# Optimization experiments

Measured on AMD Instinct MI355X. Metric: run time of the kernel, lower is better.

## Reference

```python
import jax, jax.numpy as jnp
import numpy as np

B, S, D, H, A = 4, 2048, 512, 8, 64


def setup_inputs() -> dict:
    key = jax.random.key(0)
    ks = jax.random.split(key, 12)
    inv_d = 1.0 / np.sqrt(D)
    inv_ha = 1.0 / np.sqrt(H * A)
    return {
        "query": jax.random.normal(ks[0], (B, S, D), jnp.float32),
        "key": jax.random.normal(ks[1], (B, S, D), jnp.float32),
        "value": jax.random.normal(ks[2], (B, S, D), jnp.float32),
        # stacked per-head projection weights, layout [H, in, out] so y = x @ W + b
        "Wq": jax.random.uniform(ks[3], (H, D, A), jnp.float32, -inv_d, inv_d),
        "bq": jax.random.uniform(ks[4], (H, A), jnp.float32, -inv_d, inv_d),
        "Wk": jax.random.uniform(ks[5], (H, D, A), jnp.float32, -inv_d, inv_d),
        "bk": jax.random.uniform(ks[6], (H, A), jnp.float32, -inv_d, inv_d),
        "Wv": jax.random.uniform(ks[7], (H, D, A), jnp.float32, -inv_d, inv_d),
        "bv": jax.random.uniform(ks[8], (H, A), jnp.float32, -inv_d, inv_d),
        "Wo": jax.random.uniform(ks[9], (H * A, D), jnp.float32, -inv_ha, inv_ha),
        "bo": jax.random.uniform(ks[10], (D,), jnp.float32, -inv_ha, inv_ha),
    }


def reference(query, key, value, Wq, bq, Wk, bk, Wv, bv, Wo, bo):
    b, s, _ = query.shape
    h, _, a = Wq.shape
    # per-head projections, batched across heads: [B,H,S,A]
    q = jnp.einsum("bsd,hda->bhsa", query, Wq) + bq[None, :, None, :]
    k = jnp.einsum("bsd,hda->bhsa", key, Wk) + bk[None, :, None, :]
    v = jnp.einsum("bsd,hda->bhsa", value, Wv) + bv[None, :, None, :]
    scale = a ** 0.5
    scores = jnp.einsum("bhqa,bhka->bhqk", q, k) / scale  # [B,H,S,S]
    # Faithful to original: subsequent_mask has 0.0 on lower tri, -inf above;
    # masked_fill(mask == 0, -1e9) therefore masks the LOWER triangle (incl diag).
    tril = jnp.tril(jnp.ones((s, s), dtype=bool))
    scores = jnp.where(tril, jnp.float32(-1e9), scores)
    attn = jax.nn.softmax(scores, axis=-1)
    out = jnp.einsum("bhqk,bhka->bhqa", attn, v)  # [B,H,S,A]
    # concat heads in order (head-major in feature dim, matching torch.cat dim=-1)
    out = out.transpose(0, 2, 1, 3).reshape(b, s, h * a)
    return out @ Wo + bo
```

## Files before the change

kernel.cpp:

```cpp
#include <hip/hip_runtime.h>
#include <hip/hip_bf16.h>

#define B_ 4
#define S_ 2048
#define D_ 512
#define H_ 8
#define A_ 64

typedef __attribute__((ext_vector_type(8))) __bf16 bf16x8;
typedef __attribute__((ext_vector_type(4))) __bf16 bf16x4;
typedef __attribute__((ext_vector_type(4))) float f32x4;

static __device__ __forceinline__ f32x4 mfma16(bf16x8 a, bf16x8 b, f32x4 c) {
  return __builtin_amdgcn_mfma_f32_16x16x32_bf16(a, b, c, 0, 0, 0);
}

static __device__ __forceinline__ f32x4 zero4() {
  f32x4 z = {0.f, 0.f, 0.f, 0.f};
  return z;
}

#define QSCALE 0.18033688011f

#if __has_builtin(__builtin_amdgcn_exp2f)
#define EXP2(x) __builtin_amdgcn_exp2f(x)
#else
#define EXP2(x) exp2f(x)
#endif

#define GLDS(g, l)                                                      \
  __builtin_amdgcn_global_load_lds(                                     \
      (const __attribute__((address_space(1))) void*)(g),               \
      (__attribute__((address_space(3))) void*)(l), 16, 0, 0)

__global__ void prep_all_kernel(const float* __restrict__ q, const float* __restrict__ k,
                                const float* __restrict__ v,
                                const float* __restrict__ Wq, const float* __restrict__ Wk,
                                const float* __restrict__ Wv, const float* __restrict__ Wo,
                                __bf16* __restrict__ xq, __bf16* __restrict__ xk,
                                __bf16* __restrict__ xv,
                                __bf16* __restrict__ tq, __bf16* __restrict__ tk,
                                __bf16* __restrict__ tv, __bf16* __restrict__ to_) {
  __shared__ float tile[64][65];
  if (blockIdx.x < 12288) {
    int idx = blockIdx.x * 256 + threadIdx.x;
    int which = idx >> 20;
    int i = idx & ((1 << 20) - 1);
    const float4* s = (const float4*)(which == 0 ? q : (which == 1 ? k : v));
    __bf16* d = (which == 0) ? xq : (which == 1 ? xk : xv);
    float4 f = s[i];
    bf16x4 o;
    o.x = (__bf16)f.x; o.y = (__bf16)f.y; o.z = (__bf16)f.z; o.w = (__bf16)f.w;
    *(bf16x4*)(d + 4 * i) = o;
  } else {
    int t = blockIdx.x - 12288;
    if (t < 192) {
      int mat = t >> 6;
      int h = (t >> 3) & 7;
      int d0 = (t & 7) * 64;
      const float* W = (mat == 0) ? Wq : (mat == 1 ? Wk : Wv);
      __bf16* dst = (mat == 0) ? tq : (mat == 1 ? tk : tv);
      float sc = (mat == 0) ? QSCALE : 1.0f;
      int a = threadIdx.x & 63, r0 = threadIdx.x >> 6;
#pragma unroll
      for (int i = 0; i < 16; i++) {
        int dd = r0 * 16 + i;
        tile[dd][a] = W[(h * D_ + d0 + dd) * A_ + a] * sc;
      }
      __syncthreads();
      int dd = threadIdx.x & 63, a0 = threadIdx.x >> 6;
#pragma unroll
      for (int i = 0; i < 16; i++) {
        int a2 = a0 * 16 + i;
        dst[(h * 64 + a2) * D_ + d0 + dd] = (__bf16)tile[dd][a2];
      }
    } else {
      int t2 = t - 192;
      int f0 = (t2 >> 3) * 64, d0 = (t2 & 7) * 64;
      int d = threadIdx.x & 63, r0 = threadIdx.x >> 6;
#pragma unroll
      for (int i = 0; i < 16; i++) {
        int ff = r0 * 16 + i;
        tile[ff][d] = Wo[(f0 + ff) * D_ + d0 + d];
      }
      __syncthreads();
      int f = threadIdx.x & 63, a0 = threadIdx.x >> 6;
#pragma unroll
      for (int i = 0; i < 16; i++) {
        int dd = a0 * 16 + i;
        to_[(d0 + dd) * D_ + f0 + f] = (__bf16)tile[f][dd];
      }
    }
  }
}

__global__ __launch_bounds__(256) void proj_gemm_kernel(
    const __bf16* __restrict__ Xq, const __bf16* __restrict__ Xk, const __bf16* __restrict__ Xv,
    const __bf16* __restrict__ Wtq, const __bf16* __restrict__ Wtk, const __bf16* __restrict__ Wtv,
    const float* __restrict__ bq, const float* __restrict__ bk, const float* __restrict__ bv,
    __bf16* __restrict__ Qb, __bf16* __restrict__ Kb, __bf16* __restrict__ Vtb) {
  int z = blockIdx.z;
  const __bf16* X  = (z == 0) ? Xq  : (z == 1 ? Xk  : Xv);
  const __bf16* Wt = (z == 0) ? Wtq : (z == 1 ? Wtk : Wtv);
  const float* bias = (z == 0) ? bq : (z == 1 ? bk : bv);
  float bscale = (z == 0) ? QSCALE : 1.0f;

  int lane = threadIdx.x & 63, wv = threadIdx.x >> 6;
  int wr = wv >> 1, wc = wv & 1;
  int quad = lane >> 4, lc = lane & 15;
  int M0 = blockIdx.x * 128, N0 = blockIdx.y * 128;
  int m0 = M0 + wr * 64, n0 = N0 + wc * 64;

  __shared__ __align__(16) __bf16 smem[2 * 2 * 128 * 64];
#define AB(buf) (smem + (buf) * 16384)
#define BB(buf) (smem + (buf) * 16384 + 8192)

  int srow = lane >> 3;
  int sg = ((lane & 7) ^ srow) * 8;

#pragma unroll
  for (int i = 0; i < 4; ++i) {
    int r0 = wv * 32 + i * 8;
    GLDS(X  + (M0 + r0 + srow) * D_ + sg, AB(0) + r0 * 64);
    GLDS(Wt + (N0 + r0 + srow) * D_ + sg, BB(0) + r0 * 64);
  }

  f32x4 acc[4][4];
#pragma unroll
  for (int mt = 0; mt < 4; mt++)
#pragma unroll
    for (int nt = 0; nt < 4; nt++) acc[mt][nt] = zero4();

  __syncthreads();

  for (int j = 0; j < 8; ++j) {
    int cb = j & 1;
    if (j < 7) {
      int k0 = (j + 1) * 64;
#pragma unroll
      for (int i = 0; i < 4; ++i) {
        int r0 = wv * 32 + i * 8;
        GLDS(X  + (M0 + r0 + srow) * D_ + k0 + sg, AB(cb ^ 1) + r0 * 64);
        GLDS(Wt + (N0 + r0 + srow) * D_ + k0 + sg, BB(cb ^ 1) + r0 * 64);
      }
    }
    const __bf16* Al = AB(cb);
    const __bf16* Bl = BB(cb);
#pragma unroll
    for (int kk = 0; kk < 2; ++kk) {
      int gp = ((kk * 4 + quad) ^ (lc & 7)) * 8;
      bf16x8 a[4], bb[4];
#pragma unroll
      for (int mt = 0; mt < 4; mt++)
        a[mt] = *(const bf16x8*)(Al + (wr * 64 + mt * 16 + lc) * 64 + gp);
#pragma unroll
      for (int nt = 0; nt < 4; nt++)
        bb[nt] = *(const bf16x8*)(Bl + (wc * 64 + nt * 16 + lc) * 64 + gp);
#pragma unroll
      for (int mt = 0; mt < 4; mt++)
#pragma unroll
        for (int nt = 0; nt < 4; nt++)
          acc[mt][nt] = mfma16(a[mt], bb[nt], acc[mt][nt]);
    }
    __syncthreads();
  }

  __bf16* vlds = smem + wv * (64 * 72);

  int h = n0 >> 6;
  int b = m0 >> 11, s0 = m0 & (S_ - 1);
  if (z < 2) {
#pragma unroll
    for (int nt = 0; nt < 4; nt++) {
      int col = n0 + nt * 16 + lc;
      float bval = bias[col] * bscale;
#pragma unroll
      for (int mt = 0; mt < 4; mt++)
#pragma unroll
        for (int r = 0; r < 4; r++)
          vlds[(mt * 16 + quad * 4 + r) * 72 + nt * 16 + lc] = (__bf16)(acc[mt][nt][r] + bval);
    }
    __asm__ volatile("s_waitcnt lgkmcnt(0)" ::: "memory");
    __bf16* dst = (z == 0) ? Qb : Kb;
#pragma unroll
    for (int it = 0; it < 8; it++) {
      int row = it * 8 + (lane >> 3);
      int c8 = (lane & 7) * 8;
      bf16x8 vv = *(const bf16x8*)(vlds + row * 72 + c8);
      *(bf16x8*)(dst + ((b * H_ + h) * S_ + s0 + row) * A_ + c8) = vv;
    }
  } else {
#pragma unroll
    for (int nt = 0; nt < 4; nt++) {
      int col = n0 + nt * 16 + lc;
      float bval = bias[col];
#pragma unroll
      for (int mt = 0; mt < 4; mt++) {
        bf16x4 pk;
#pragma unroll
        for (int r = 0; r < 4; r++) pk[r] = (__bf16)(acc[mt][nt][r] + bval);
        *(bf16x4*)(vlds + (nt * 16 + lc) * 72 + mt * 16 + quad * 4) = pk;
      }
    }
    __asm__ volatile("s_waitcnt lgkmcnt(0)" ::: "memory");
#pragma unroll
    for (int it = 0; it < 8; it++) {
      int a_l = it * 8 + (lane >> 3);
      int s_l = (lane & 7) * 8;
      bf16x8 vvv = *(const bf16x8*)(vlds + a_l * 72 + s_l);
      *(bf16x8*)(Vtb + ((b * H_ + h) * A_ + a_l) * S_ + s0 + s_l) = vvv;
    }
  }
}

__global__ __launch_bounds__(256) void flash_kernel(const __bf16* __restrict__ Q,
                                                    const __bf16* __restrict__ K,
                                                    const __bf16* __restrict__ Vt,
                                                    __bf16* __restrict__ O) {
  int id = blockIdx.x;
  int xcd = id & 7, slot = id >> 3;
  int half = slot >> 5;
  int p = (slot >> 2) & 7;
  int bh = xcd * 4 + (slot & 3);
  int lane = threadIdx.x & 63, wv = threadIdx.x >> 6;
  int quad = lane >> 4, lc = lane & 15;
  int R1 = p * 128 + half * 64 + wv * 16;
  int R2 = (15 - p) * 128 + half * 64 + wv * 16;
  int t0 = 2 * p + half, ntile = 32 - t0;

  const __bf16* Qp = Q + bh * S_ * A_;
  const __bf16* Kp = K + bh * S_ * A_;
  const __bf16* Vp = Vt + bh * A_ * S_;

  __shared__ __align__(16) __bf16 kvbuf[2][2][64][64];
  __shared__ __align__(16) __bf16 plds_all[4][16][72];
  __bf16* plds = &plds_all[wv][0][0];

  int srow = lane >> 3;
  int sg = ((lane & 7) ^ srow) * 8;
  int wr16 = wv * 16;

  {
    int kt = t0 << 6;
#pragma unroll
    for (int i = 0; i < 2; ++i) {
      int r0 = wr16 + i * 8;
      GLDS(Kp + (kt + r0 + srow) * A_ + sg, &kvbuf[0][0][r0][0]);
      GLDS(Vp + (r0 + srow) * S_ + kt + sg, &kvbuf[0][1][r0][0]);
    }
  }

  bf16x8 qf1[2], qf2[2];
  qf1[0] = *(const bf16x8*)(Qp + (R1 + lc) * A_ + quad * 8);
  qf1[1] = *(const bf16x8*)(Qp + (R1 + lc) * A_ + 32 + quad * 8);
  qf2[0] = *(const bf16x8*)(Qp + (R2 + lc) * A_ + quad * 8);
  qf2[1] = *(const bf16x8*)(Qp + (R2 + lc) * A_ + 32 + quad * 8);

  f32x4 o1[4], o2[4];
  float ls1 = 0.f, ls2 = 0.f;
#pragma unroll
  for (int t = 0; t < 4; t++) { o1[t] = zero4(); o2[t] = zero4(); }

  int g0 = (quad ^ (lc & 7)) * 8;
  int g1 = ((quad + 4) ^ (lc & 7)) * 8;

  __syncthreads();

  for (int j = 0; j < ntile; ++j) {
    int t = t0 + j;
    int cb = j & 1;
    if (j + 1 < ntile) {
      int ktn = (t + 1) << 6;
#pragma unroll
      for (int i = 0; i < 2; ++i) {
        int r0 = wr16 + i * 8;
        GLDS(Kp + (ktn + r0 + srow) * A_ + sg, &kvbuf[cb ^ 1][0][r0][0]);
        GLDS(Vp + (r0 + srow) * S_ + ktn + sg, &kvbuf[cb ^ 1][1][r0][0]);
      }
    }
    const __bf16* Kl = &kvbuf[cb][0][0][0];
    const __bf16* Vl = &kvbuf[cb][1][0][0];
    bool g2 = (t * 64 + 63 > R2);

    bf16x8 kf[4][2], vf[4][2];
#pragma unroll
    for (int nt = 0; nt < 4; nt++) {
      int rr = nt * 16 + lc;
      kf[nt][0] = *(const bf16x8*)(Kl + rr * 64 + g0);
      kf[nt][1] = *(const bf16x8*)(Kl + rr * 64 + g1);
    }
#pragma unroll
    for (int ot = 0; ot < 4; ot++) {
      int rr = ot * 16 + lc;
      vf[ot][0] = *(const bf16x8*)(Vl + rr * 64 + g0);
      vf[ot][1] = *(const bf16x8*)(Vl + rr * 64 + g1);
    }

    f32x4 sc[4];
#pragma unroll
    for (int nt = 0; nt < 4; nt++) {
      f32x4 ss = zero4();
      ss = mfma16(kf[nt][0], qf1[0], ss);
      ss = mfma16(kf[nt][1], qf1[1], ss);
      sc[nt] = ss;
    }
    if (t * 64 <= R1 + 15) {
      int row = R1 + lc;
#pragma unroll
      for (int nt = 0; nt < 4; nt++)
#pragma unroll
        for (int r = 0; r < 4; r++) {
          int col = t * 64 + nt * 16 + quad * 4 + r;
          float pv = (col <= row) ? 0.0f : EXP2(sc[nt][r]);
          ls1 += pv;
          sc[nt][r] = pv;
        }
    } else {
#pragma unroll
      for (int nt = 0; nt < 4; nt++)
#pragma unroll
        for (int r = 0; r < 4; r++) {
          float pv = EXP2(sc[nt][r]);
          ls1 += pv;
          sc[nt][r] = pv;
        }
    }
#pragma unroll
    for (int nt = 0; nt < 4; nt++) {
      bf16x4 pk;
#pragma unroll
      for (int r = 0; r < 4; r++) pk[r] = (__bf16)sc[nt][r];
      *(bf16x4*)(plds + lc * 72 + nt * 16 + quad * 4) = pk;
    }
    f32x4 sc2[4];
    if (g2) {
#pragma unroll
      for (int nt = 0; nt < 4; nt++) {
        f32x4 ss = zero4();
        ss = mfma16(kf[nt][0], qf2[0], ss);
        ss = mfma16(kf[nt][1], qf2[1], ss);
        sc2[nt] = ss;
      }
    }
    __asm__ volatile("s_waitcnt lgkmcnt(0)" ::: "memory");
    {
      bf16x8 pf0 = *(const bf16x8*)(plds + lc * 72 + quad * 8);
      bf16x8 pf1 = *(const bf16x8*)(plds + lc * 72 + 32 + quad * 8);
      __builtin_amdgcn_s_setprio(1);
#pragma unroll
      for (int ot = 0; ot < 4; ot++) {
        o1[ot] = mfma16(pf0, vf[ot][0], o1[ot]);
        o1[ot] = mfma16(pf1, vf[ot][1], o1[ot]);
      }
      __builtin_amdgcn_s_setprio(0);
    }

    if (g2) {
      if (t * 64 <= R2 + 15) {
        int row = R2 + lc;
#pragma unroll
        for (int nt = 0; nt < 4; nt++)
#pragma unroll
          for (int r = 0; r < 4; r++) {
            int col = t * 64 + nt * 16 + quad * 4 + r;
            float pv = (col <= row) ? 0.0f : EXP2(sc2[nt][r]);
            ls2 += pv;
            sc2[nt][r] = pv;
          }
      } else {
#pragma unroll
        for (int nt = 0; nt < 4; nt++)
#pragma unroll
          for (int r = 0; r < 4; r++) {
            float pv = EXP2(sc2[nt][r]);
            ls2 += pv;
            sc2[nt][r] = pv;
          }
      }
#pragma unroll
      for (int nt = 0; nt < 4; nt++) {
        bf16x4 pk;
#pragma unroll
        for (int r = 0; r < 4; r++) pk[r] = (__bf16)sc2[nt][r];
        *(bf16x4*)(plds + lc * 72 + nt * 16 + quad * 4) = pk;
      }
      __asm__ volatile("s_waitcnt lgkmcnt(0)" ::: "memory");
      bf16x8 pf0 = *(const bf16x8*)(plds + lc * 72 + quad * 8);
      bf16x8 pf1 = *(const bf16x8*)(plds + lc * 72 + 32 + quad * 8);
      __builtin_amdgcn_s_setprio(1);
#pragma unroll
      for (int ot = 0; ot < 4; ot++) {
        o2[ot] = mfma16(pf0, vf[ot][0], o2[ot]);
        o2[ot] = mfma16(pf1, vf[ot][1], o2[ot]);
      }
      __builtin_amdgcn_s_setprio(0);
    }
    __syncthreads();
  }

  ls1 += __shfl_xor(ls1, 16, 64);
  ls1 += __shfl_xor(ls1, 32, 64);
  ls2 += __shfl_xor(ls2, 16, 64);
  ls2 += __shfl_xor(ls2, 32, 64);
  float rl1[4], rl2[4];
#pragma unroll
  for (int r = 0; r < 4; r++) {
    rl1[r] = 1.0f / __shfl(ls1, quad * 4 + r, 64);
    rl2[r] = 1.0f / __shfl(ls2, quad * 4 + r, 64);
  }

  int b = bh >> 3, h = bh & 7;

#pragma unroll
  for (int r = 0; r < 4; r++)
#pragma unroll
    for (int ot = 0; ot < 4; ot++)
      plds[(quad * 4 + r) * 72 + ot * 16 + lc] = (__bf16)(o1[ot][r] * rl1[r]);
  __asm__ volatile("s_waitcnt lgkmcnt(0)" ::: "memory");
#pragma unroll
  for (int it = 0; it < 2; it++) {
    int row = it * 8 + (lane >> 3);
    int c8 = (lane & 7) * 8;
    *(bf16x8*)(O + (b * S_ + R1 + row) * (H_ * A_) + h * 64 + c8) =
        *(const bf16x8*)(plds + row * 72 + c8);
  }

#pragma unroll
  for (int r = 0; r < 4; r++)
#pragma unroll
    for (int ot = 0; ot < 4; ot++)
      plds[(quad * 4 + r) * 72 + ot * 16 + lc] = (__bf16)(o2[ot][r] * rl2[r]);
  __asm__ volatile("s_waitcnt lgkmcnt(0)" ::: "memory");
#pragma unroll
  for (int it = 0; it < 2; it++) {
    int row = it * 8 + (lane >> 3);
    int c8 = (lane & 7) * 8;
    int grow = R2 + row;
    if (grow != S_ - 1)
      *(bf16x8*)(O + (b * S_ + grow) * (H_ * A_) + h * 64 + c8) =
          *(const bf16x8*)(plds + row * 72 + c8);
  }

  if (p == 7 && half == 0) {
    int a = threadIdx.x >> 2;
    int li = threadIdx.x & 3;
    const __bf16* src = Vp + a * S_;
    float ssum = 0.f;
#pragma unroll 8
    for (int j2 = 0; j2 < 64; j2++) {
      bf16x8 vv = *(const bf16x8*)(src + (j2 * 4 + li) * 8);
#pragma unroll
      for (int e = 0; e < 8; e++) ssum += (float)vv[e];
    }
    ssum += __shfl_xor(ssum, 1, 64);
    ssum += __shfl_xor(ssum, 2, 64);
    if (li == 0)
      O[(b * S_ + (S_ - 1)) * (H_ * A_) + h * 64 + a] = (__bf16)(ssum * (1.0f / 2048.0f));
  }
}

__global__ __launch_bounds__(256) void out_gemm_kernel(const __bf16* __restrict__ Ob,
                                                       const __bf16* __restrict__ Wot,
                                                       const float* __restrict__ bo,
                                                       float* __restrict__ out) {
  int lane = threadIdx.x & 63, wv = threadIdx.x >> 6;
  int wr = wv >> 1, wc = wv & 1;
  int quad = lane >> 4, lc = lane & 15;
  int M0 = blockIdx.x * 128, N0 = blockIdx.y * 128;
  int m0 = M0 + wr * 64, n0 = N0 + wc * 64;

  __shared__ __align__(16) __bf16 smem[2 * 2 * 128 * 64];

  int srow = lane >> 3;
  int sg = ((lane & 7) ^ srow) * 8;

#pragma unroll
  for (int i = 0; i < 4; ++i) {
    int r0 = wv * 32 + i * 8;
    GLDS(Ob  + (M0 + r0 + srow) * D_ + sg, AB(0) + r0 * 64);
    GLDS(Wot + (N0 + r0 + srow) * D_ + sg, BB(0) + r0 * 64);
  }

  f32x4 acc[4][4];
#pragma unroll
  for (int mt = 0; mt < 4; mt++)
#pragma unroll
    for (int nt = 0; nt < 4; nt++) acc[mt][nt] = zero4();

  __syncthreads();

  for (int j = 0; j < 8; ++j) {
    int cb = j & 1;
    if (j < 7) {
      int k0 = (j + 1) * 64;
#pragma unroll
      for (int i = 0; i < 4; ++i) {
        int r0 = wv * 32 + i * 8;
        GLDS(Ob  + (M0 + r0 + srow) * D_ + k0 + sg, AB(cb ^ 1) + r0 * 64);
        GLDS(Wot + (N0 + r0 + srow) * D_ + k0 + sg, BB(cb ^ 1) + r0 * 64);
      }
    }
    const __bf16* Al = AB(cb);
    const __bf16* Bl = BB(cb);
#pragma unroll
    for (int kk = 0; kk < 2; ++kk) {
      int gp = ((kk * 4 + quad) ^ (lc & 7)) * 8;
      bf16x8 a[4], bb[4];
#pragma unroll
      for (int mt = 0; mt < 4; mt++)
        a[mt] = *(const bf16x8*)(Al + (wr * 64 + mt * 16 + lc) * 64 + gp);
#pragma unroll
      for (int nt = 0; nt < 4; nt++)
        bb[nt] = *(const bf16x8*)(Bl + (wc * 64 + nt * 16 + lc) * 64 + gp);
#pragma unroll
      for (int mt = 0; mt < 4; mt++)
#pragma unroll
        for (int nt = 0; nt < 4; nt++)
          acc[mt][nt] = mfma16(a[mt], bb[nt], acc[mt][nt]);
    }
    __syncthreads();
  }

#pragma unroll
  for (int nt = 0; nt < 4; nt++) {
    int col = n0 + nt * 16 + lc;
    float bval = bo[col];
#pragma unroll
    for (int mt = 0; mt < 4; mt++)
#pragma unroll
      for (int r = 0; r < 4; r++) {
        int row = m0 + mt * 16 + quad * 4 + r;
        out[row * D_ + col] = acc[mt][nt][r] + bval;
      }
  }
}

extern "C" void kernel_launch(void* const* d_in, const int* in_sizes, int n_in,
                              void* d_out, int out_size, void* d_ws, size_t ws_size,
                              hipStream_t stream) {
  const float* q  = (const float*)d_in[0];
  const float* k  = (const float*)d_in[1];
  const float* v  = (const float*)d_in[2];
  const float* Wq = (const float*)d_in[3];
  const float* bq = (const float*)d_in[4];
  const float* Wk = (const float*)d_in[5];
  const float* bk = (const float*)d_in[6];
  const float* Wv = (const float*)d_in[7];
  const float* bv = (const float*)d_in[8];
  const float* Wo = (const float*)d_in[9];
  const float* bo = (const float*)d_in[10];

  char* ws = (char*)d_ws;
  __bf16* Xq  = (__bf16*)(ws + 0);
  __bf16* Xk  = (__bf16*)(ws + 8388608);
  __bf16* Xv  = (__bf16*)(ws + 16777216);
  __bf16* Wtq = (__bf16*)(ws + 25165824);
  __bf16* Wtk = (__bf16*)(ws + 25690112);
  __bf16* Wtv = (__bf16*)(ws + 26214400);
  __bf16* Wot = (__bf16*)(ws + 26738688);
  __bf16* Qb  = (__bf16*)(ws + 27262976);
  __bf16* Kb  = (__bf16*)(ws + 35651584);
  __bf16* Vtb = (__bf16*)(ws + 44040192);
  __bf16* Ob  = (__bf16*)(ws + 52428800);

  prep_all_kernel<<<12544, 256, 0, stream>>>(q, k, v, Wq, Wk, Wv, Wo,
                                             Xq, Xk, Xv, Wtq, Wtk, Wtv, Wot);
  proj_gemm_kernel<<<dim3(64, 4, 3), 256, 0, stream>>>(Xq, Xk, Xv, Wtq, Wtk, Wtv,
                                                       bq, bk, bv, Qb, Kb, Vtb);
  flash_kernel<<<dim3(512), 256, 0, stream>>>(Qb, Kb, Vtb, Ob);
  out_gemm_kernel<<<dim3(64, 4), 256, 0, stream>>>(Ob, Wot, bo, (float*)d_out);
}
```

Measured before the change: 173.4 us.

## Fuse fp32-to-bf16 input conversion into projection GEMM A-tile loads

```diff
diff --git a/kernel.cpp b/kernel.cpp
--- a/kernel.cpp
+++ b/kernel.cpp
@@ -33,74 +33,58 @@
       (const __attribute__((address_space(1))) void*)(g),               \
       (__attribute__((address_space(3))) void*)(l), 16, 0, 0)
 
-__global__ void prep_all_kernel(const float* __restrict__ q, const float* __restrict__ k,
-                                const float* __restrict__ v,
-                                const float* __restrict__ Wq, const float* __restrict__ Wk,
+__global__ void prep_all_kernel(const float* __restrict__ Wq, const float* __restrict__ Wk,
                                 const float* __restrict__ Wv, const float* __restrict__ Wo,
-                                __bf16* __restrict__ xq, __bf16* __restrict__ xk,
-                                __bf16* __restrict__ xv,
                                 __bf16* __restrict__ tq, __bf16* __restrict__ tk,
                                 __bf16* __restrict__ tv, __bf16* __restrict__ to_) {
   __shared__ float tile[64][65];
-  if (blockIdx.x < 12288) {
-    int idx = blockIdx.x * 256 + threadIdx.x;
-    int which = idx >> 20;
-    int i = idx & ((1 << 20) - 1);
-    const float4* s = (const float4*)(which == 0 ? q : (which == 1 ? k : v));
-    __bf16* d = (which == 0) ? xq : (which == 1 ? xk : xv);
-    float4 f = s[i];
-    bf16x4 o;
-    o.x = (__bf16)f.x; o.y = (__bf16)f.y; o.z = (__bf16)f.z; o.w = (__bf16)f.w;
-    *(bf16x4*)(d + 4 * i) = o;
+  int t = blockIdx.x;
+  if (t < 192) {
+    int mat = t >> 6;
+    int h = (t >> 3) & 7;
+    int d0 = (t & 7) * 64;
+    const float* W = (mat == 0) ? Wq : (mat == 1 ? Wk : Wv);
+    __bf16* dst = (mat == 0) ? tq : (mat == 1 ? tk : tv);
+    float sc = (mat == 0) ? QSCALE : 1.0f;
+    int a = threadIdx.x & 63, r0 = threadIdx.x >> 6;
+#pragma unroll
+    for (int i = 0; i < 16; i++) {
+      int dd = r0 * 16 + i;
+      tile[dd][a] = W[(h * D_ + d0 + dd) * A_ + a] * sc;
+    }
+    __syncthreads();
+    int dd = threadIdx.x & 63, a0 = threadIdx.x >> 6;
+#pragma unroll
+    for (int i = 0; i < 16; i++) {
+      int a2 = a0 * 16 + i;
+      dst[(h * 64 + a2) * D_ + d0 + dd] = (__bf16)tile[dd][a2];
+    }
   } else {
-    int t = blockIdx.x - 12288;
-    if (t < 192) {
-      int mat = t >> 6;
-      int h = (t >> 3) & 7;
-      int d0 = (t & 7) * 64;
-      const float* W = (mat == 0) ? Wq : (mat == 1 ? Wk : Wv);
-      __bf16* dst = (mat == 0) ? tq : (mat == 1 ? tk : tv);
-      float sc = (mat == 0) ? QSCALE : 1.0f;
-      int a = threadIdx.x & 63, r0 = threadIdx.x >> 6;
-#pragma unroll
-      for (int i = 0; i < 16; i++) {
-        int dd = r0 * 16 + i;
-        tile[dd][a] = W[(h * D_ + d0 + dd) * A_ + a] * sc;
-      }
-      __syncthreads();
-      int dd = threadIdx.x & 63, a0 = threadIdx.x >> 6;
-#pragma unroll
-      for (int i = 0; i < 16; i++) {
-        int a2 = a0 * 16 + i;
-        dst[(h * 64 + a2) * D_ + d0 + dd] = (__bf16)tile[dd][a2];
-      }
-    } else {
-      int t2 = t - 192;
-      int f0 = (t2 >> 3) * 64, d0 = (t2 & 7) * 64;
-      int d = threadIdx.x & 63, r0 = threadIdx.x >> 6;
-#pragma unroll
-      for (int i = 0; i < 16; i++) {
-        int ff = r0 * 16 + i;
-        tile[ff][d] = Wo[(f0 + ff) * D_ + d0 + d];
-      }
-      __syncthreads();
-      int f = threadIdx.x & 63, a0 = threadIdx.x >> 6;
-#pragma unroll
-      for (int i = 0; i < 16; i++) {
-        int dd = a0 * 16 + i;
-        to_[(d0 + dd) * D_ + f0 + f] = (__bf16)tile[f][dd];
-      }
+    int t2 = t - 192;
+    int f0 = (t2 >> 3) * 64, d0 = (t2 & 7) * 64;
+    int d = threadIdx.x & 63, r0 = threadIdx.x >> 6;
+#pragma unroll
+    for (int i = 0; i < 16; i++) {
+      int ff = r0 * 16 + i;
+      tile[ff][d] = Wo[(f0 + ff) * D_ + d0 + d];
+    }
+    __syncthreads();
+    int f = threadIdx.x & 63, a0 = threadIdx.x >> 6;
+#pragma unroll
+    for (int i = 0; i < 16; i++) {
+      int dd = a0 * 16 + i;
+      to_[(d0 + dd) * D_ + f0 + f] = (__bf16)tile[f][dd];
     }
   }
 }
 
 __global__ __launch_bounds__(256) void proj_gemm_kernel(
-    const __bf16* __restrict__ Xq, const __bf16* __restrict__ Xk, const __bf16* __restrict__ Xv,
+    const float* __restrict__ q, const float* __restrict__ k, const float* __restrict__ v,
     const __bf16* __restrict__ Wtq, const __bf16* __restrict__ Wtk, const __bf16* __restrict__ Wtv,
     const float* __restrict__ bq, const float* __restrict__ bk, const float* __restrict__ bv,
     __bf16* __restrict__ Qb, __bf16* __restrict__ Kb, __bf16* __restrict__ Vtb) {
   int z = blockIdx.z;
-  const __bf16* X  = (z == 0) ? Xq  : (z == 1 ? Xk  : Xv);
+  const float* X = (z == 0) ? q : (z == 1 ? k : v);
   const __bf16* Wt = (z == 0) ? Wtq : (z == 1 ? Wtk : Wtv);
   const float* bias = (z == 0) ? bq : (z == 1 ? bk : bv);
   float bscale = (z == 0) ? QSCALE : 1.0f;
@@ -117,13 +101,37 @@
 
   int srow = lane >> 3;
   int sg = ((lane & 7) ^ srow) * 8;
-
+  int g8 = (lane & 7) * 8;
+
+  float4 fv[4][2];
+#define LOAD_A(k0)                                                          \
+  {                                                                          \
+    _Pragma("unroll") for (int i = 0; i < 4; ++i) {                          \
+      const float* src = X + (M0 + wv * 32 + i * 8 + srow) * D_ + (k0) + g8; \
+      fv[i][0] = *(const float4*)(src);                                      \
+      fv[i][1] = *(const float4*)(src + 4);                                  \
+    }                                                                        \
+  }
+#define WRITE_A(buf)                                                         \
+  {                                                                          \
+    _Pragma("unroll") for (int i = 0; i < 4; ++i) {                          \
+      int row = wv * 32 + i * 8 + srow;                                      \
+      bf16x8 tt;                                                             \
+      tt[0] = (__bf16)fv[i][0].x; tt[1] = (__bf16)fv[i][0].y;                \
+      tt[2] = (__bf16)fv[i][0].z; tt[3] = (__bf16)fv[i][0].w;                \
+      tt[4] = (__bf16)fv[i][1].x; tt[5] = (__bf16)fv[i][1].y;                \
+      tt[6] = (__bf16)fv[i][1].z; tt[7] = (__bf16)fv[i][1].w;                \
+      *(bf16x8*)(AB(buf) + row * 64 + sg) = tt;                              \
+    }                                                                        \
+  }
+
+  LOAD_A(0);
 #pragma unroll
   for (int i = 0; i < 4; ++i) {
     int r0 = wv * 32 + i * 8;
-    GLDS(X  + (M0 + r0 + srow) * D_ + sg, AB(0) + r0 * 64);
     GLDS(Wt + (N0 + r0 + srow) * D_ + sg, BB(0) + r0 * 64);
   }
+  WRITE_A(0);
 
   f32x4 acc[4][4];
 #pragma unroll
@@ -140,9 +148,9 @@
 #pragma unroll
       for (int i = 0; i < 4; ++i) {
         int r0 = wv * 32 + i * 8;
-        GLDS(X  + (M0 + r0 + srow) * D_ + k0 + sg, AB(cb ^ 1) + r0 * 64);
         GLDS(Wt + (N0 + r0 + srow) * D_ + k0 + sg, BB(cb ^ 1) + r0 * 64);
       }
+      LOAD_A(k0);
     }
     const __bf16* Al = AB(cb);
     const __bf16* Bl = BB(cb);
@@ -162,6 +170,7 @@
         for (int nt = 0; nt < 4; nt++)
           acc[mt][nt] = mfma16(a[mt], bb[nt], acc[mt][nt]);
     }
+    if (j < 7) WRITE_A(cb ^ 1);
     __syncthreads();
   }
 
@@ -551,9 +560,6 @@
   const float* bo = (const float*)d_in[10];
 
   char* ws = (char*)d_ws;
-  __bf16* Xq  = (__bf16*)(ws + 0);
-  __bf16* Xk  = (__bf16*)(ws + 8388608);
-  __bf16* Xv  = (__bf16*)(ws + 16777216);
   __bf16* Wtq = (__bf16*)(ws + 25165824);
   __bf16* Wtk = (__bf16*)(ws + 25690112);
   __bf16* Wtv = (__bf16*)(ws + 26214400);
@@ -563,9 +569,8 @@
   __bf16* Vtb = (__bf16*)(ws + 44040192);
   __bf16* Ob  = (__bf16*)(ws + 52428800);
 
-  prep_all_kernel<<<12544, 256, 0, stream>>>(q, k, v, Wq, Wk, Wv, Wo,
-                                             Xq, Xk, Xv, Wtq, Wtk, Wtv, Wot);
-  proj_gemm_kernel<<<dim3(64, 4, 3), 256, 0, stream>>>(Xq, Xk, Xv, Wtq, Wtk, Wtv,
+  prep_all_kernel<<<256, 256, 0, stream>>>(Wq, Wk, Wv, Wo, Wtq, Wtk, Wtv, Wot);
+  proj_gemm_kernel<<<dim3(64, 4, 3), 256, 0, stream>>>(q, k, v, Wtq, Wtk, Wtv,
                                                        bq, bk, bv, Qb, Kb, Vtb);
   flash_kernel<<<dim3(512), 256, 0, stream>>>(Qb, Kb, Vtb, Ob);
   out_gemm_kernel<<<dim3(64, 4), 256, 0, stream>>>(Ob, Wot, bo, (float*)d_out);
```

Measured after the change: 179.9 us. +3.7%, slower.
